# Optimization experiments

Measured on AMD Instinct MI355X. Metric: run time of the kernel, lower is better.

The kernel has to match this reference:

```python
import jax, jax.numpy as jnp
import numpy as np

EMBED = 768
N_HEADS = 12
HEAD = EMBED // N_HEADS  # 64
B, T = 2, 2048


def setup_inputs() -> dict:
    key = jax.random.key(0)
    ks = jax.random.split(key, 5)
    s = 0.02
    return {
        "x": jax.random.normal(ks[0], (B, T, EMBED), dtype=jnp.float32),
        "w_attn": jax.random.normal(ks[1], (EMBED, 3 * EMBED), dtype=jnp.float32) * s,
        "b_attn": jnp.zeros((3 * EMBED,), dtype=jnp.float32),
        "w_proj": jax.random.normal(ks[2], (EMBED, EMBED), dtype=jnp.float32) * s,
        "b_proj": jnp.zeros((EMBED,), dtype=jnp.float32),
    }


def reference(x, w_attn, b_attn, w_proj, b_proj):
    b, t, c = x.shape
    scale = HEAD ** -0.5
    qkv = x @ w_attn + b_attn  # [b,t,3c]
    q, k, v = jnp.split(qkv, 3, axis=-1)

    # einops 'b t (h n) -> b n t h' with n=N_HEADS: channel dim factors as
    # (head_size, n_heads) — head index is the inner factor.
    def split_heads(u):
        return u.reshape(b, t, HEAD, N_HEADS).transpose(0, 3, 1, 2)  # [b,n,t,h]

    q, k, v = split_heads(q), split_heads(k), split_heads(v)

    scores = jnp.einsum("bnth,bnsh->bnts", q, k) * scale  # [b,n,t,t]
    causal = jnp.tril(jnp.ones((t, t), dtype=bool))
    scores = jnp.where(causal, scores, jnp.finfo(scores.dtype).min)
    weights = jax.nn.softmax(scores, axis=-1)
    att = jnp.einsum("bnts,bnsh->bnth", weights, v)  # [b,n,t,h]

    # 'b n t h -> b t (n h)': heads are the OUTER factor on output
    att = att.transpose(0, 2, 1, 3).reshape(b, t, c)
    return att @ w_proj + b_proj
```

## Files before the change

### kernel.cpp

```cpp
#include <hip/hip_runtime.h>
#include <hip/hip_bf16.h>
#include <math.h>

#define NB      2
#define T_SZ    2048
#define EMBEDC  768
#define NHEADS  12
#define HEADD   64
#define QKV_PER (NB * NHEADS * T_SZ * HEADD)
#define QSCALE  0.18033688011112042f

typedef __bf16 bf16x8 __attribute__((ext_vector_type(8)));
typedef float  f32x4  __attribute__((ext_vector_type(4)));

__device__ inline ushort f2bf(float x) {
    union { float f; uint u; } v; v.f = x;
    uint r = v.u + 0x7fffu + ((v.u >> 16) & 1u);
    return (ushort)(r >> 16);
}

__device__ inline void gload16(const ushort* g, ushort* l) {
    __builtin_amdgcn_global_load_lds(
        (const __attribute__((address_space(1))) unsigned int*)g,
        (__attribute__((address_space(3))) unsigned int*)l, 16, 0, 0);
}

__global__ __launch_bounds__(256) void cast_k(const float* __restrict__ in,
                                              ushort* __restrict__ out, int n)
{
    int i = (blockIdx.x * 256 + threadIdx.x) * 8;
    if (i >= n) return;
    float4 a = *(const float4*)(in + i);
    float4 b = *(const float4*)(in + i + 4);
    union { ushort u[8]; int4 v; } p;
    p.u[0] = f2bf(a.x); p.u[1] = f2bf(a.y); p.u[2] = f2bf(a.z); p.u[3] = f2bf(a.w);
    p.u[4] = f2bf(b.x); p.u[5] = f2bf(b.y); p.u[6] = f2bf(b.z); p.u[7] = f2bf(b.w);
    *(int4*)(out + i) = p.v;
}

template <int PERM>
__global__ __launch_bounds__(256) void tcast_k(const float* __restrict__ in,
                                               ushort* __restrict__ out,
                                               int R, int C)
{
    __shared__ float t[32][33];
    const int c0 = blockIdx.x * 32, r0 = blockIdx.y * 32;
    const int tx = threadIdx.x & 31, ty = threadIdx.x >> 5;
#pragma unroll
    for (int u = 0; u < 4; ++u)
        t[ty + 8 * u][tx] = in[(size_t)(r0 + ty + 8 * u) * C + c0 + tx];
    __syncthreads();
#pragma unroll
    for (int u = 0; u < 4; ++u) {
        int n = c0 + ty + 8 * u;
        int orow = n;
        if (PERM) {
            int mat = n / EMBEDC, cc = n % EMBEDC;
            orow = mat * EMBEDC + (cc % NHEADS) * HEADD + cc / NHEADS;
        }
        out[(size_t)orow * R + r0 + tx] = f2bf(t[tx][ty + 8 * u]);
    }
}

__global__ __launch_bounds__(256) void vt_k(const ushort* __restrict__ in,
                                            ushort* __restrict__ out)
{
    __shared__ ushort tile[64][66];
    const int bh = blockIdx.y;
    const int t0 = blockIdx.x * 64;
    const int tid = threadIdx.x;
#pragma unroll
    for (int u = 0; u < 2; ++u) {
        int s = tid + 256 * u;
        int r = s >> 3, c8 = s & 7;
        *(bf16x8*)&tile[r][c8 * 8] =
            *(const bf16x8*)(in + ((size_t)bh * T_SZ + t0 + r) * HEADD + c8 * 8);
    }
    __syncthreads();
#pragma unroll
    for (int u = 0; u < 2; ++u) {
        int s = tid + 256 * u;
        int hd = s >> 3, tt = s & 7;
        union { ushort v[8]; int4 q; } pk;
#pragma unroll
        for (int j = 0; j < 8; ++j) pk.v[j] = tile[tt * 8 + j][hd];
        *(int4*)(out + ((size_t)bh * HEADD + hd) * T_SZ + t0 + tt * 8) = pk.q;
    }
}

template <int MODE>
__global__ __launch_bounds__(256) void gemm_bf16_k(
    const ushort* __restrict__ A, const ushort* __restrict__ Bt,
    const float* __restrict__ bias, void* __restrict__ outp,
    int M, int N, int K)
{
    __shared__ ushort As[128 * 32];
    __shared__ ushort Bs[128 * 32];

    const int tid = threadIdx.x;
    const int w = tid >> 6, l = tid & 63;
    const int g = l >> 4, r16 = l & 15;
    const int wr = w >> 1, wc = w & 1;
    const int m0 = blockIdx.y * 128, n0 = blockIdx.x * 128;

    const int srow = l >> 2;
    const int sc = ((l & 3) ^ (srow & 3)) * 8;
    const ushort* gA0 = A + (size_t)(m0 + 32 * w + srow) * K + sc;
    const ushort* gA1 = gA0 + (size_t)16 * K;
    const ushort* gB0 = Bt + (size_t)(n0 + 32 * w + srow) * K + sc;
    const ushort* gB1 = gB0 + (size_t)16 * K;
    ushort* lA0 = &As[(32 * w) * 32];
    ushort* lA1 = &As[(32 * w + 16) * 32];
    ushort* lB0 = &Bs[(32 * w) * 32];
    ushort* lB1 = &Bs[(32 * w + 16) * 32];

    f32x4 acc[4][4];
#pragma unroll
    for (int i = 0; i < 4; ++i)
#pragma unroll
        for (int j = 0; j < 4; ++j) acc[i][j] = (f32x4){0.f, 0.f, 0.f, 0.f};

    const int rck = (r16 & 3);

    for (int k0 = 0; k0 < K; k0 += 32) {
        gload16(gA0 + k0, lA0);
        gload16(gA1 + k0, lA1);
        gload16(gB0 + k0, lB0);
        gload16(gB1 + k0, lB1);
        __syncthreads();

        bf16x8 af[4], bfr[4];
#pragma unroll
        for (int ms = 0; ms < 4; ++ms) {
            int row = 64 * wr + 16 * ms + r16;
            af[ms] = *(const bf16x8*)&As[row * 32 + ((g ^ rck) * 8)];
        }
#pragma unroll
        for (int ns = 0; ns < 4; ++ns) {
            int row = 64 * wc + 16 * ns + r16;
            bfr[ns] = *(const bf16x8*)&Bs[row * 32 + ((g ^ rck) * 8)];
        }
        __builtin_amdgcn_s_setprio(1);
#pragma unroll
        for (int ms = 0; ms < 4; ++ms)
#pragma unroll
            for (int ns = 0; ns < 4; ++ns)
                acc[ms][ns] = __builtin_amdgcn_mfma_f32_16x16x32_bf16(
                    af[ms], bfr[ns], acc[ms][ns], 0, 0, 0);
        __builtin_amdgcn_s_setprio(0);
        __syncthreads();
    }

#pragma unroll
    for (int ns = 0; ns < 4; ++ns) {
        const int n = n0 + 64 * wc + 16 * ns + r16;
        if (MODE == 0) {
            float* out = (float*)outp;
            const float bv = bias[n];
#pragma unroll
            for (int ms = 0; ms < 4; ++ms) {
                const int mb = m0 + 64 * wr + 16 * ms + 4 * g;
#pragma unroll
                for (int r = 0; r < 4; ++r)
                    out[(size_t)(mb + r) * N + n] = acc[ms][ns][r] + bv;
            }
        } else {
            ushort* ob = (ushort*)outp;
            const int mat  = n / EMBEDC;
            const int c    = n - mat * EMBEDC;
            const int head = c >> 6;
            const int hd   = c & 63;
            const float bv = bias[mat * EMBEDC + hd * NHEADS + head];
            const float qs = (mat == 0) ? QSCALE : 1.f;
#pragma unroll
            for (int ms = 0; ms < 4; ++ms) {
                const int mb = m0 + 64 * wr + 16 * ms + 4 * g;
#pragma unroll
                for (int r = 0; r < 4; ++r) {
                    const int m = mb + r;
                    const int b = m >> 11, t = m & 2047;
                    const size_t bh = (size_t)(b * NHEADS + head);
                    ob[(size_t)mat * QKV_PER + (bh * T_SZ + t) * HEADD + hd] =
                        f2bf((acc[ms][ns][r] + bv) * qs);
                }
            }
        }
    }
}

__global__ __launch_bounds__(256) void attn_mfma_k(
    const ushort* __restrict__ Qb, const ushort* __restrict__ Kb,
    const ushort* __restrict__ Vtb, ushort* __restrict__ Out)
{
    __shared__ ushort Ks[64 * 64];
    __shared__ ushort Vs[64 * 64];

    const int qb = blockIdx.x;
    const int bh = blockIdx.y;
    const int bb = bh / NHEADS, head = bh % NHEADS;
    const int tid = threadIdx.x;
    const int w = tid >> 6, l = tid & 63;
    const int g = l >> 4, r16 = l & 15;
    const int q0 = qb * 64;
    const ushort* Kg = Kb + (size_t)bh * T_SZ * HEADD;
    const ushort* Vg = Vtb + (size_t)bh * HEADD * T_SZ;

    bf16x8 qf[2];
    {
        const ushort* qp = Qb + (size_t)bh * T_SZ * HEADD +
                           (size_t)(q0 + 16 * w + r16) * HEADD + g * 8;
        qf[0] = *(const bf16x8*)(qp);
        qf[1] = *(const bf16x8*)(qp + 32);
    }

    f32x4 o[4];
#pragma unroll
    for (int dc = 0; dc < 4; ++dc) o[dc] = (f32x4){0.f, 0.f, 0.f, 0.f};
    float mR = -1e30f, lR = 0.f;

    bf16x8 kr[2], vr[2];
#pragma unroll
    for (int u = 0; u < 2; ++u) {
        int f = tid + 256 * u; int row = f >> 3, c8 = f & 7;
        kr[u] = *(const bf16x8*)(Kg + (size_t)row * HEADD + c8 * 8);
        vr[u] = *(const bf16x8*)(Vg + (size_t)row * T_SZ + c8 * 8);
    }
#pragma unroll
    for (int u = 0; u < 2; ++u) {
        int f = tid + 256 * u; int row = f >> 3, c8 = f & 7;
        int dst = ((c8 ^ (row & 7)) * 8);
        *(bf16x8*)&Ks[row * 64 + dst] = kr[u];
        *(bf16x8*)&Vs[row * 64 + dst] = vr[u];
    }
    __syncthreads();

    for (int kt = 0; kt <= qb; ++kt) {
        if (kt < qb) {
            const int k1 = (kt + 1) * 64;
#pragma unroll
            for (int u = 0; u < 2; ++u) {
                int f = tid + 256 * u; int row = f >> 3, c8 = f & 7;
                kr[u] = *(const bf16x8*)(Kg + (size_t)(k1 + row) * HEADD + c8 * 8);
                vr[u] = *(const bf16x8*)(Vg + (size_t)row * T_SZ + k1 + c8 * 8);
            }
        }

        f32x4 st[4];
        __builtin_amdgcn_s_setprio(1);
#pragma unroll
        for (int kc = 0; kc < 4; ++kc) {
            int row = kc * 16 + r16;
            const ushort* krow = &Ks[row * 64];
            bf16x8 a0 = *(const bf16x8*)(krow + ((g    ) ^ (row & 7)) * 8);
            bf16x8 a1 = *(const bf16x8*)(krow + ((g + 4) ^ (row & 7)) * 8);
            f32x4 c = (f32x4){0.f, 0.f, 0.f, 0.f};
            c = __builtin_amdgcn_mfma_f32_16x16x32_bf16(a0, qf[0], c, 0, 0, 0);
            c = __builtin_amdgcn_mfma_f32_16x16x32_bf16(a1, qf[1], c, 0, 0, 0);
            st[kc] = c;
        }
        __builtin_amdgcn_s_setprio(0);

        if (kt == qb) {
            const int qloc = 16 * w + r16;
#pragma unroll
            for (int kc = 0; kc < 4; ++kc)
#pragma unroll
                for (int r = 0; r < 4; ++r)
                    if (kc * 16 + 4 * g + r > qloc) st[kc][r] = -1e30f;
        }

        float pm = -1e30f;
#pragma unroll
        for (int kc = 0; kc < 4; ++kc)
#pragma unroll
            for (int r = 0; r < 4; ++r) pm = fmaxf(pm, st[kc][r]);
        pm = fmaxf(pm, __shfl_xor(pm, 16));
        pm = fmaxf(pm, __shfl_xor(pm, 32));
        float mNew = fmaxf(mR, pm);
        float sc = exp2f(mR - mNew);
        float p[16];
        float rs = 0.f;
#pragma unroll
        for (int kc = 0; kc < 4; ++kc)
#pragma unroll
            for (int r = 0; r < 4; ++r) {
                float e = exp2f(st[kc][r] - mNew);
                p[kc * 4 + r] = e;
                rs += e;
            }
        rs += __shfl_xor(rs, 16);
        rs += __shfl_xor(rs, 32);
        lR = lR * sc + rs;
        mR = mNew;
#pragma unroll
        for (int dc = 0; dc < 4; ++dc) o[dc] *= sc;

        uint pk[4][2];
#pragma unroll
        for (int kc = 0; kc < 4; ++kc) {
            pk[kc][0] = (uint)f2bf(p[kc * 4 + 0]) | ((uint)f2bf(p[kc * 4 + 1]) << 16);
            pk[kc][1] = (uint)f2bf(p[kc * 4 + 2]) | ((uint)f2bf(p[kc * 4 + 3]) << 16);
        }

        const int srcLo = ((g & 1) << 5) | r16;
        const int srcHi = srcLo + 16;
        const bool hiSel = (g >> 1) != 0;
        bf16x8 pb[2];
#pragma unroll
        for (int s = 0; s < 2; ++s) {
            uint A0 = (uint)__shfl((int)pk[2 * s][0],     srcLo);
            uint A1 = (uint)__shfl((int)pk[2 * s][1],     srcLo);
            uint B0 = (uint)__shfl((int)pk[2 * s + 1][0], srcLo);
            uint B1 = (uint)__shfl((int)pk[2 * s + 1][1], srcLo);
            uint A2 = (uint)__shfl((int)pk[2 * s][0],     srcHi);
            uint A3 = (uint)__shfl((int)pk[2 * s][1],     srcHi);
            uint B2 = (uint)__shfl((int)pk[2 * s + 1][0], srcHi);
            uint B3 = (uint)__shfl((int)pk[2 * s + 1][1], srcHi);
            union { uint u[4]; bf16x8 v; } t;
            t.u[0] = hiSel ? B0 : A0;
            t.u[1] = hiSel ? B1 : A1;
            t.u[2] = hiSel ? B2 : A2;
            t.u[3] = hiSel ? B3 : A3;
            pb[s] = t.v;
        }

        __builtin_amdgcn_s_setprio(1);
#pragma unroll
        for (int dc = 0; dc < 4; ++dc) {
            int row = dc * 16 + r16;
            const ushort* vrow = &Vs[row * 64];
            bf16x8 v0 = *(const bf16x8*)(vrow + ((g    ) ^ (row & 7)) * 8);
            bf16x8 v1 = *(const bf16x8*)(vrow + ((g + 4) ^ (row & 7)) * 8);
            o[dc] = __builtin_amdgcn_mfma_f32_16x16x32_bf16(v0, pb[0], o[dc], 0, 0, 0);
            o[dc] = __builtin_amdgcn_mfma_f32_16x16x32_bf16(v1, pb[1], o[dc], 0, 0, 0);
        }
        __builtin_amdgcn_s_setprio(0);

        __syncthreads();
        if (kt < qb) {
#pragma unroll
            for (int u = 0; u < 2; ++u) {
                int f = tid + 256 * u; int row = f >> 3, c8 = f & 7;
                int dst = ((c8 ^ (row & 7)) * 8);
                *(bf16x8*)&Ks[row * 64 + dst] = kr[u];
                *(bf16x8*)&Vs[row * 64 + dst] = vr[u];
            }
            __syncthreads();
        }
    }

    const float inv = 1.f / lR;
    const int q = q0 + 16 * w + r16;
    ushort* orow = Out + ((size_t)(bb * T_SZ + q)) * EMBEDC + head * HEADD;
#pragma unroll
    for (int dc = 0; dc < 4; ++dc)
#pragma unroll
        for (int r = 0; r < 4; ++r)
            orow[dc * 16 + 4 * g + r] = f2bf(o[dc][r] * inv);
}

extern "C" void kernel_launch(void* const* d_in, const int* in_sizes, int n_in,
                              void* d_out, int out_size, void* d_ws, size_t ws_size,
                              hipStream_t stream)
{
    const float* x      = (const float*)d_in[0];
    const float* w_attn = (const float*)d_in[1];
    const float* b_attn = (const float*)d_in[2];
    const float* w_proj = (const float*)d_in[3];
    const float* b_proj = (const float*)d_in[4];
    float* out = (float*)d_out;

    ushort* qw   = (ushort*)d_ws;
    ushort* vT   = qw + (size_t)3 * QKV_PER;
    ushort* attb = vT + QKV_PER;
    ushort* xb   = attb + QKV_PER;
    ushort* waT  = xb + QKV_PER;
    ushort* wpT  = waT + (size_t)EMBEDC * 3 * EMBEDC;

    cast_k<<<QKV_PER / (256 * 8), 256, 0, stream>>>(x, xb, QKV_PER);
    tcast_k<1><<<dim3(3 * EMBEDC / 32, EMBEDC / 32), 256, 0, stream>>>(
        w_attn, waT, EMBEDC, 3 * EMBEDC);
    tcast_k<0><<<dim3(EMBEDC / 32, EMBEDC / 32), 256, 0, stream>>>(
        w_proj, wpT, EMBEDC, EMBEDC);

    gemm_bf16_k<1><<<dim3(2304 / 128, 4096 / 128), 256, 0, stream>>>(
        xb, waT, b_attn, qw, NB * T_SZ, 3 * EMBEDC, EMBEDC);

    vt_k<<<dim3(T_SZ / 64, NB * NHEADS), 256, 0, stream>>>(
        qw + 2 * (size_t)QKV_PER, vT);

    attn_mfma_k<<<dim3(T_SZ / 64, NB * NHEADS), 256, 0, stream>>>(
        qw, qw + QKV_PER, vT, attb);

    gemm_bf16_k<0><<<dim3(768 / 128, 4096 / 128), 256, 0, stream>>>(
        attb, wpT, b_proj, out, NB * T_SZ, EMBEDC, EMBEDC);
}
```

Measured before the change: 138.0 us.

## Double-buffer GEMM LDS tiles and widen attention KV tiles with lazy rescale

```diff
diff --git a/kernel.cpp b/kernel.cpp
--- a/kernel.cpp
+++ b/kernel.cpp
@@ -17,6 +17,12 @@
     union { float f; uint u; } v; v.f = x;
     uint r = v.u + 0x7fffu + ((v.u >> 16) & 1u);
     return (ushort)(r >> 16);
+}
+
+__device__ inline uint pack2bf(float a, float b) {
+    union { __bf16 h[2]; uint u; } t;
+    t.h[0] = (__bf16)a; t.h[1] = (__bf16)b;
+    return t.u;
 }
 
 __device__ inline void gload16(const ushort* g, ushort* l) {
@@ -88,14 +94,22 @@
     }
 }
 
+#define STAGE(buf, koff)                                        \
+    do {                                                        \
+        gload16(gA0 + (koff), &As[buf][lA0o]);                  \
+        gload16(gA1 + (koff), &As[buf][lA1o]);                  \
+        gload16(gB0 + (koff), &Bs[buf][lB0o]);                  \
+        gload16(gB1 + (koff), &Bs[buf][lB1o]);                  \
+    } while (0)
+
 template <int MODE>
 __global__ __launch_bounds__(256) void gemm_bf16_k(
     const ushort* __restrict__ A, const ushort* __restrict__ Bt,
     const float* __restrict__ bias, void* __restrict__ outp,
     int M, int N, int K)
 {
-    __shared__ ushort As[128 * 32];
-    __shared__ ushort Bs[128 * 32];
+    __shared__ ushort As[2][128 * 32];
+    __shared__ ushort Bs[2][128 * 32];
 
     const int tid = threadIdx.x;
     const int w = tid >> 6, l = tid & 63;
@@ -104,15 +118,13 @@
     const int m0 = blockIdx.y * 128, n0 = blockIdx.x * 128;
 
     const int srow = l >> 2;
-    const int sc = ((l & 3) ^ (srow & 3)) * 8;
-    const ushort* gA0 = A + (size_t)(m0 + 32 * w + srow) * K + sc;
+    const int scol = ((l & 3) ^ (srow & 3)) * 8;
+    const ushort* gA0 = A + (size_t)(m0 + 32 * w + srow) * K + scol;
     const ushort* gA1 = gA0 + (size_t)16 * K;
-    const ushort* gB0 = Bt + (size_t)(n0 + 32 * w + srow) * K + sc;
+    const ushort* gB0 = Bt + (size_t)(n0 + 32 * w + srow) * K + scol;
     const ushort* gB1 = gB0 + (size_t)16 * K;
-    ushort* lA0 = &As[(32 * w) * 32];
-    ushort* lA1 = &As[(32 * w + 16) * 32];
-    ushort* lB0 = &Bs[(32 * w) * 32];
-    ushort* lB1 = &Bs[(32 * w + 16) * 32];
+    const int lA0o = (32 * w) * 32,      lA1o = (32 * w + 16) * 32;
+    const int lB0o = lA0o,               lB1o = lA1o;
 
     f32x4 acc[4][4];
 #pragma unroll
@@ -122,33 +134,35 @@
 
     const int rck = (r16 & 3);
 
+    STAGE(0, 0);
+    __syncthreads();
+
+    int cur = 0;
     for (int k0 = 0; k0 < K; k0 += 32) {
-        gload16(gA0 + k0, lA0);
-        gload16(gA1 + k0, lA1);
-        gload16(gB0 + k0, lB0);
-        gload16(gB1 + k0, lB1);
-        __syncthreads();
-
+        if (k0 + 32 < K) STAGE(cur ^ 1, k0 + 32);
+
+        const ushort* sA = As[cur];
+        const ushort* sB = Bs[cur];
         bf16x8 af[4], bfr[4];
 #pragma unroll
         for (int ms = 0; ms < 4; ++ms) {
             int row = 64 * wr + 16 * ms + r16;
-            af[ms] = *(const bf16x8*)&As[row * 32 + ((g ^ rck) * 8)];
+            af[ms] = *(const bf16x8*)&sA[row * 32 + ((g ^ rck) * 8)];
         }
 #pragma unroll
         for (int ns = 0; ns < 4; ++ns) {
             int row = 64 * wc + 16 * ns + r16;
-            bfr[ns] = *(const bf16x8*)&Bs[row * 32 + ((g ^ rck) * 8)];
-        }
-        __builtin_amdgcn_s_setprio(1);
+            bfr[ns] = *(const bf16x8*)&sB[row * 32 + ((g ^ rck) * 8)];
+        }
 #pragma unroll
         for (int ms = 0; ms < 4; ++ms)
 #pragma unroll
             for (int ns = 0; ns < 4; ++ns)
                 acc[ms][ns] = __builtin_amdgcn_mfma_f32_16x16x32_bf16(
                     af[ms], bfr[ns], acc[ms][ns], 0, 0, 0);
-        __builtin_amdgcn_s_setprio(0);
+
         __syncthreads();
+        cur ^= 1;
     }
 
 #pragma unroll
@@ -188,12 +202,12 @@
     }
 }
 
-__global__ __launch_bounds__(256) void attn_mfma_k(
+__global__ __launch_bounds__(256, 3) void attn_mfma_k(
     const ushort* __restrict__ Qb, const ushort* __restrict__ Kb,
     const ushort* __restrict__ Vtb, ushort* __restrict__ Out)
 {
-    __shared__ ushort Ks[64 * 64];
-    __shared__ ushort Vs[64 * 64];
+    __shared__ ushort Ks[128 * 64];
+    __shared__ ushort Vs[64 * 128];
 
     const int qb = blockIdx.x;
     const int bh = blockIdx.y;
@@ -202,7 +216,8 @@
     const int w = tid >> 6, l = tid & 63;
     const int g = l >> 4, r16 = l & 15;
     const int q0 = qb * 64;
-    const ushort* Kg = Kb + (size_t)bh * T_SZ * HEADD;
+    const int nt = qb / 2 + 1;
+    const ushort* Kg = Qb ? Kb + (size_t)bh * T_SZ * HEADD : nullptr;
     const ushort* Vg = Vtb + (size_t)bh * HEADD * T_SZ;
 
     bf16x8 qf[2];
@@ -218,37 +233,44 @@
     for (int dc = 0; dc < 4; ++dc) o[dc] = (f32x4){0.f, 0.f, 0.f, 0.f};
     float mR = -1e30f, lR = 0.f;
 
-    bf16x8 kr[2], vr[2];
-#pragma unroll
-    for (int u = 0; u < 2; ++u) {
-        int f = tid + 256 * u; int row = f >> 3, c8 = f & 7;
-        kr[u] = *(const bf16x8*)(Kg + (size_t)row * HEADD + c8 * 8);
-        vr[u] = *(const bf16x8*)(Vg + (size_t)row * T_SZ + c8 * 8);
-    }
-#pragma unroll
-    for (int u = 0; u < 2; ++u) {
-        int f = tid + 256 * u; int row = f >> 3, c8 = f & 7;
-        int dst = ((c8 ^ (row & 7)) * 8);
-        *(bf16x8*)&Ks[row * 64 + dst] = kr[u];
-        *(bf16x8*)&Vs[row * 64 + dst] = vr[u];
+    bf16x8 kr[4], vr[4];
+#pragma unroll
+    for (int u = 0; u < 4; ++u) {
+        int s = tid + 256 * u;
+        kr[u] = *(const bf16x8*)(Kg + (size_t)(s >> 3) * HEADD + (s & 7) * 8);
+        vr[u] = *(const bf16x8*)(Vg + (size_t)(s >> 4) * T_SZ + (s & 15) * 8);
+    }
+#pragma unroll
+    for (int u = 0; u < 4; ++u) {
+        int s = tid + 256 * u;
+        int krow = s >> 3, kc8 = s & 7;
+        int vrow = s >> 4, vc16 = s & 15;
+        *(bf16x8*)&Ks[krow * 64 + ((kc8 ^ (krow & 7)) * 8)] = kr[u];
+        *(bf16x8*)&Vs[vrow * 128 + ((vc16 ^ (vrow & 15)) * 8)] = vr[u];
     }
     __syncthreads();
 
-    for (int kt = 0; kt <= qb; ++kt) {
-        if (kt < qb) {
-            const int k1 = (kt + 1) * 64;
-#pragma unroll
-            for (int u = 0; u < 2; ++u) {
-                int f = tid + 256 * u; int row = f >> 3, c8 = f & 7;
-                kr[u] = *(const bf16x8*)(Kg + (size_t)(k1 + row) * HEADD + c8 * 8);
-                vr[u] = *(const bf16x8*)(Vg + (size_t)row * T_SZ + k1 + c8 * 8);
-            }
-        }
-
-        f32x4 st[4];
-        __builtin_amdgcn_s_setprio(1);
-#pragma unroll
-        for (int kc = 0; kc < 4; ++kc) {
+    const int srcLo = ((g & 1) << 5) | r16;
+    const int srcHi = srcLo + 16;
+    const bool hiSel = (g >> 1) != 0;
+    const int qg = q0 + 16 * w + r16;
+
+    for (int kt = 0; kt < nt; ++kt) {
+        if (kt + 1 < nt) {
+            const int k1 = (kt + 1) * 128;
+#pragma unroll
+            for (int u = 0; u < 4; ++u) {
+                int s = tid + 256 * u;
+                kr[u] = *(const bf16x8*)(Kg + (size_t)(k1 + (s >> 3)) * HEADD +
+                                         (s & 7) * 8);
+                vr[u] = *(const bf16x8*)(Vg + (size_t)(s >> 4) * T_SZ + k1 +
+                                         (s & 15) * 8);
+            }
+        }
+
+        f32x4 st[8];
+#pragma unroll
+        for (int kc = 0; kc < 8; ++kc) {
             int row = kc * 16 + r16;
             const ushort* krow = &Ks[row * 64];
             bf16x8 a0 = *(const bf16x8*)(krow + ((g    ) ^ (row & 7)) * 8);
@@ -258,56 +280,53 @@
             c = __builtin_amdgcn_mfma_f32_16x16x32_bf16(a1, qf[1], c, 0, 0, 0);
             st[kc] = c;
         }
-        __builtin_amdgcn_s_setprio(0);
-
-        if (kt == qb) {
-            const int qloc = 16 * w + r16;
-#pragma unroll
-            for (int kc = 0; kc < 4; ++kc)
+
+        if (kt == nt - 1) {
+            const int k0 = kt * 128;
+#pragma unroll
+            for (int kc = 0; kc < 8; ++kc)
 #pragma unroll
                 for (int r = 0; r < 4; ++r)
-                    if (kc * 16 + 4 * g + r > qloc) st[kc][r] = -1e30f;
+                    if (k0 + kc * 16 + 4 * g + r > qg) st[kc][r] = -1e30f;
         }
 
         float pm = -1e30f;
 #pragma unroll
-        for (int kc = 0; kc < 4; ++kc)
+        for (int kc = 0; kc < 8; ++kc)
 #pragma unroll
             for (int r = 0; r < 4; ++r) pm = fmaxf(pm, st[kc][r]);
         pm = fmaxf(pm, __shfl_xor(pm, 16));
         pm = fmaxf(pm, __shfl_xor(pm, 32));
-        float mNew = fmaxf(mR, pm);
-        float sc = exp2f(mR - mNew);
-        float p[16];
+        if (!__all(pm - mR <= 8.f)) {
+            float mNew = fmaxf(mR, pm);
+            float sc = exp2f(mR - mNew);
+            lR *= sc;
+#pragma unroll
+            for (int dc = 0; dc < 4; ++dc) o[dc] *= sc;
+            mR = mNew;
+        }
         float rs = 0.f;
 #pragma unroll
-        for (int kc = 0; kc < 4; ++kc)
+        for (int kc = 0; kc < 8; ++kc)
 #pragma unroll
             for (int r = 0; r < 4; ++r) {
-                float e = exp2f(st[kc][r] - mNew);
-                p[kc * 4 + r] = e;
+                float e = exp2f(st[kc][r] - mR);
+                st[kc][r] = e;
                 rs += e;
             }
         rs += __shfl_xor(rs, 16);
         rs += __shfl_xor(rs, 32);
-        lR = lR * sc + rs;
-        mR = mNew;
-#pragma unroll
-        for (int dc = 0; dc < 4; ++dc) o[dc] *= sc;
-
-        uint pk[4][2];
-#pragma unroll
-        for (int kc = 0; kc < 4; ++kc) {
-            pk[kc][0] = (uint)f2bf(p[kc * 4 + 0]) | ((uint)f2bf(p[kc * 4 + 1]) << 16);
-            pk[kc][1] = (uint)f2bf(p[kc * 4 + 2]) | ((uint)f2bf(p[kc * 4 + 3]) << 16);
-        }
-
-        const int srcLo = ((g & 1) << 5) | r16;
-        const int srcHi = srcLo + 16;
-        const bool hiSel = (g >> 1) != 0;
-        bf16x8 pb[2];
-#pragma unroll
-        for (int s = 0; s < 2; ++s) {
+        lR += rs;
+
+        uint pk[8][2];
+#pragma unroll
+        for (int kc = 0; kc < 8; ++kc) {
+            pk[kc][0] = pack2bf(st[kc][0], st[kc][1]);
+            pk[kc][1] = pack2bf(st[kc][2], st[kc][3]);
+        }
+
+#pragma unroll
+        for (int s = 0; s < 4; ++s) {
             uint A0 = (uint)__shfl((int)pk[2 * s][0],     srcLo);
             uint A1 = (uint)__shfl((int)pk[2 * s][1],     srcLo);
             uint B0 = (uint)__shfl((int)pk[2 * s + 1][0], srcLo);
@@ -321,37 +340,32 @@
             t.u[1] = hiSel ? B1 : A1;
             t.u[2] = hiSel ? B2 : A2;
             t.u[3] = hiSel ? B3 : A3;
-            pb[s] = t.v;
-        }
-
-        __builtin_amdgcn_s_setprio(1);
-#pragma unroll
-        for (int dc = 0; dc < 4; ++dc) {
-            int row = dc * 16 + r16;
-            const ushort* vrow = &Vs[row * 64];
-            bf16x8 v0 = *(const bf16x8*)(vrow + ((g    ) ^ (row & 7)) * 8);
-            bf16x8 v1 = *(const bf16x8*)(vrow + ((g + 4) ^ (row & 7)) * 8);
-            o[dc] = __builtin_amdgcn_mfma_f32_16x16x32_bf16(v0, pb[0], o[dc], 0, 0, 0);
-            o[dc] = __builtin_amdgcn_mfma_f32_16x16x32_bf16(v1, pb[1], o[dc], 0, 0, 0);
-        }
-        __builtin_amdgcn_s_setprio(0);
+#pragma unroll
+            for (int dc = 0; dc < 4; ++dc) {
+                int row = dc * 16 + r16;
+                bf16x8 vf = *(const bf16x8*)
+                    &Vs[row * 128 + (((4 * s + g) ^ (row & 15)) * 8)];
+                o[dc] = __builtin_amdgcn_mfma_f32_16x16x32_bf16(
+                    vf, t.v, o[dc], 0, 0, 0);
+            }
+        }
 
         __syncthreads();
-        if (kt < qb) {
-#pragma unroll
-            for (int u = 0; u < 2; ++u) {
-                int f = tid + 256 * u; int row = f >> 3, c8 = f & 7;
-                int dst = ((c8 ^ (row & 7)) * 8);
-                *(bf16x8*)&Ks[row * 64 + dst] = kr[u];
-                *(bf16x8*)&Vs[row * 64 + dst] = vr[u];
+        if (kt + 1 < nt) {
+#pragma unroll
+            for (int u = 0; u < 4; ++u) {
+                int s = tid + 256 * u;
+                int krow = s >> 3, kc8 = s & 7;
+                int vrow = s >> 4, vc16 = s & 15;
+                *(bf16x8*)&Ks[krow * 64 + ((kc8 ^ (krow & 7)) * 8)] = kr[u];
+                *(bf16x8*)&Vs[vrow * 128 + ((vc16 ^ (vrow & 15)) * 8)] = vr[u];
             }
             __syncthreads();
         }
     }
 
     const float inv = 1.f / lR;
-    const int q = q0 + 16 * w + r16;
-    ushort* orow = Out + ((size_t)(bb * T_SZ + q)) * EMBEDC + head * HEADD;
+    ushort* orow = Out + ((size_t)(bb * T_SZ + qg)) * EMBEDC + head * HEADD;
 #pragma unroll
     for (int dc = 0; dc < 4; ++dc)
 #pragma unroll
```

Result: faster. 131.4 us (-4.8%).
